# Optimization experiments

Measured on AMD Instinct MI355X. Metric: run time of the kernel, lower is better.

Reference implementation:

```python
import jax, jax.numpy as jnp
import numpy as np

NB, NA, NC, NH, NW = 32, 5, 20, 76, 76
MAXT, NGT_PER_IMG = 50, 12
ANCHORS = [1.3221, 1.73145, 3.19275, 4.00944, 5.05587, 8.09892, 9.47112, 4.84053, 11.2364, 10.0071]
NOOBJ_SCALE, OBJ_SCALE = 1.0, 5.0
COORD_SCALE, CLASS_SCALE = 1.0, 1.0
SIL_THRESH = 0.6


def setup_inputs() -> dict:
    key = jax.random.key(0)
    output = jax.random.normal(key, (NB, NA * (5 + NC), NH, NW), jnp.float32) * 0.5
    rng = np.random.default_rng(0)
    tgt = np.zeros((NB, MAXT * 5), np.float32)
    for b in range(NB):
        # distinct grid cells per image -> scatter order never matters
        cells = rng.choice(NH * NW, size=NGT_PER_IMG, replace=False)
        gj, gi = cells // NW, cells % NW
        tgt[b, 0:NGT_PER_IMG * 5:5] = rng.integers(0, NC, NGT_PER_IMG)
        tgt[b, 1:NGT_PER_IMG * 5:5] = (gi + rng.uniform(0.1, 0.9, NGT_PER_IMG)) / NW
        tgt[b, 2:NGT_PER_IMG * 5:5] = (gj + rng.uniform(0.1, 0.9, NGT_PER_IMG)) / NH
        tgt[b, 3:NGT_PER_IMG * 5:5] = rng.uniform(0.03, 0.3, NGT_PER_IMG)
        tgt[b, 4:NGT_PER_IMG * 5:5] = rng.uniform(0.03, 0.3, NGT_PER_IMG)
    return {"output": output, "target": jnp.asarray(tgt),
            "anchors": jnp.asarray(ANCHORS, jnp.float32)}


def _iou(a, b):
    # boxes (..., 4) in (cx, cy, w, h); matches bbox_iou(x1y1x2y2=False)
    ax, ay, aw, ah = a[..., 0], a[..., 1], a[..., 2], a[..., 3]
    bx, by, bw, bh = b[..., 0], b[..., 1], b[..., 2], b[..., 3]
    uw = jnp.maximum(ax + aw / 2, bx + bw / 2) - jnp.minimum(ax - aw / 2, bx - bw / 2)
    uh = jnp.maximum(ay + ah / 2, by + bh / 2) - jnp.minimum(ay - ah / 2, by - bh / 2)
    cw = aw + bw - uw
    ch = ah + bh - uh
    carea = jnp.where((cw <= 0) | (ch <= 0), 0.0, cw * ch)
    return carea / (aw * ah + bw * bh - carea)


def reference(output, target, anchors):
    nB, _, nH, nW = output.shape
    nA, nC = NA, NC
    T = target.shape[1] // 5
    total = nB * nA * nH * nW

    out = output.reshape(nB, nA, 5 + nC, nH, nW)
    x = jax.nn.sigmoid(out[:, :, 0])          # [nB,nA,nH,nW]
    y = jax.nn.sigmoid(out[:, :, 1])
    w = out[:, :, 2]
    h = out[:, :, 3]
    conf = jax.nn.sigmoid(out[:, :, 4])
    cls_logits = jnp.moveaxis(out[:, :, 5:], 2, -1)  # [nB,nA,nH,nW,nC]

    aw, ah = anchors[0::2], anchors[1::2]     # [nA]
    px = x + jnp.arange(nW, dtype=x.dtype)[None, None, None, :]
    py = y + jnp.arange(nH, dtype=x.dtype)[None, None, :, None]
    pw = jnp.exp(w) * aw[None, :, None, None]
    ph = jnp.exp(h) * ah[None, :, None, None]
    # torch uses .data -> decoded boxes are detached
    pred = jax.lax.stop_gradient(jnp.stack([px, py, pw, ph], -1))  # [nB,nA,nH,nW,4]

    tgt = target.reshape(nB, T, 5)
    cls_t = tgt[..., 0]
    gx, gy = tgt[..., 1] * nW, tgt[..., 2] * nH
    gw, gh = tgt[..., 3] * nW, tgt[..., 4] * nH
    valid = tgt[..., 1] != 0                  # [nB,T] (padding uses x==0)
    gt_boxes = jnp.stack([gx, gy, gw, gh], -1)  # [nB,T,4]

    # --- conf_mask: zero out cells whose best-matching-gt IoU > thresh ---
    ious = _iou(pred[:, :, :, :, None, :], gt_boxes[:, None, None, None, :, :])  # [nB,nA,nH,nW,T]
    max_iou = jnp.max(jnp.where(valid[:, None, None, None, :], ious, 0.0), axis=-1)
    conf_mask = jnp.where(max_iou > SIL_THRESH, 0.0, NOOBJ_SCALE)

    # --- best anchor per gt (shape-only IoU, zero-centered) ---
    abox = jnp.stack([jnp.zeros_like(aw), jnp.zeros_like(ah), aw, ah], -1)  # [nA,4]
    gbox0 = jnp.stack([jnp.zeros_like(gw), jnp.zeros_like(gh), gw, gh], -1)
    aiou = _iou(gbox0[:, :, None, :], abox[None, None, :, :])  # [nB,T,nA]
    best_n = jnp.argmax(aiou, axis=-1)                         # first max == strict > loop

    gi = jnp.clip(gx.astype(jnp.int32), 0, nW - 1)
    gj = jnp.clip(gy.astype(jnp.int32), 0, nH - 1)
    bidx = jnp.arange(nB)[:, None]
    idx = ((bidx * nA + best_n) * nH + gj) * nW + gi
    idx = jnp.where(valid, idx, total)        # invalid -> out of range -> dropped
    idxf = idx.reshape(-1)

    aw_b, ah_b = aw[best_n], ah[best_n]
    tx_v = gx - gi
    ty_v = gy - gj
    tw_v = jnp.log(jnp.where(valid, gw, aw_b) / aw_b)
    th_v = jnp.log(jnp.where(valid, gh, ah_b) / ah_b)
    pred_flat = pred.reshape(total, 4)
    pb = pred_flat[jnp.clip(idx, 0, total - 1)]        # [nB,T,4]
    tconf_v = _iou(gt_boxes, pb)

    def scat(vals):
        return jnp.zeros((total,), x.dtype).at[idxf].set(
            vals.reshape(-1).astype(x.dtype), mode='drop').reshape(nB, nA, nH, nW)

    coord_mask = scat(jnp.ones_like(gx))
    cls_mask = scat(jnp.ones_like(gx))
    tx = scat(tx_v)
    ty = scat(ty_v)
    tw = scat(tw_v)
    th = scat(th_v)
    tconf = scat(tconf_v)
    tcls = scat(cls_t)
    conf_mask = conf_mask.reshape(-1).at[idxf].set(OBJ_SCALE, mode='drop').reshape(nB, nA, nH, nW)
    conf_mask = jnp.sqrt(conf_mask)

    cm = coord_mask
    loss_x = COORD_SCALE * jnp.sum((x * cm - tx * cm) ** 2) / 2.0
    loss_y = COORD_SCALE * jnp.sum((y * cm - ty * cm) ** 2) / 2.0
    loss_w = COORD_SCALE * jnp.sum((w * cm - tw * cm) ** 2) / 2.0
    loss_h = COORD_SCALE * jnp.sum((h * cm - th * cm) ** 2) / 2.0
    loss_conf = jnp.sum((conf * conf_mask - tconf * conf_mask) ** 2) / 2.0

    logp = jax.nn.log_softmax(cls_logits, axis=-1)
    ce = -jnp.take_along_axis(logp, tcls.astype(jnp.int32)[..., None], axis=-1)[..., 0]
    loss_cls = CLASS_SCALE * jnp.sum(ce * cls_mask)

    return (loss_x + loss_y + loss_w + loss_h + loss_conf + loss_cls) / nB
```

## Files before the change

kernel.cpp:

```cpp
#include <hip/hip_runtime.h>
#include <math.h>

#define NB 32
#define NA 5
#define NC 20
#define NH 76
#define NW 76
#define MAXT 50
#define NHW (NH * NW)
#define CH (5 + NC)
#define CELLS_PER_IMG (NA * NHW)
#define NGROUPS (CELLS_PER_IMG / 4)
#define P2_BLOCKS ((NGROUPS + 255) / 256)
#define TOTAL_BLOCKS (P2_BLOCKS * NB)
#define SIL 0.6f

__device__ __forceinline__ float sigmoidf_(float v) {
    return 1.0f / (1.0f + __expf(-v));
}

__global__ __launch_bounds__(256) void yolo_loss_kernel(
    const float* __restrict__ out, const float* __restrict__ target,
    const float* __restrict__ anchors, float* __restrict__ partials)
{
    __shared__ float  s_aw[NA], s_ah[NA];
    __shared__ float4 s_tbox[MAXT];
    __shared__ float  s_thr[MAXT];
    __shared__ float  s_bar[MAXT];
    __shared__ int    s_cell[MAXT];
    __shared__ int    s_cnt;
    __shared__ float  s_part[4];

    const int tid = threadIdx.x;
    const int b   = blockIdx.y;

    if (tid < NA) { s_aw[tid] = anchors[2 * tid]; s_ah[tid] = anchors[2 * tid + 1]; }
    if (tid == 0) s_cnt = 0;
    __syncthreads();

    float lsum = 0.0f;

    if (tid < MAXT) {
        const float* tp = target + (size_t)b * MAXT * 5 + tid * 5;
        float tc = tp[0], xn = tp[1], yn = tp[2], wn = tp[3], hn = tp[4];
        if (xn != 0.0f) {
            float gx = xn * NW, gy = yn * NH, gw = wn * NW, gh = hn * NH;

            int bn = 0; float best = -1.0f;
            #pragma unroll
            for (int a = 0; a < NA; ++a) {
                float mw = fminf(gw, s_aw[a]);
                float mh = fminf(gh, s_ah[a]);
                float car = mw * mh;
                float iou = car / (gw * gh + s_aw[a] * s_ah[a] - car);
                if (iou > best) { best = iou; bn = a; }
            }
            int gi = (int)gx; gi = gi < 0 ? 0 : (gi > NW - 1 ? NW - 1 : gi);
            int gj = (int)gy; gj = gj < 0 ? 0 : (gj > NH - 1 ? NH - 1 : gj);

            int pos = atomicAdd(&s_cnt, 1);
            float barea = gw * gh;
            s_tbox[pos] = make_float4(gx - 0.5f * gw, gy - 0.5f * gh,
                                      gx + 0.5f * gw, gy + 0.5f * gh);
            s_thr[pos]  = 0.375f * barea;
            s_bar[pos]  = barea;
            s_cell[pos] = bn * NHW + gj * NW + gi;

            if (blockIdx.x == 0) {
                float tx = gx - gi, ty = gy - gj;
                float tw = __logf(gw / s_aw[bn]);
                float th = __logf(gh / s_ah[bn]);
                const float* cp = out + ((size_t)(b * NA + bn) * CH) * NHW + gj * NW + gi;
                float xr = sigmoidf_(cp[0]);
                float yr = sigmoidf_(cp[(size_t)1 * NHW]);
                float wr = cp[(size_t)2 * NHW];
                float hr = cp[(size_t)3 * NHW];
                lsum += 0.5f * ((xr - tx) * (xr - tx) + (yr - ty) * (yr - ty) +
                                (wr - tw) * (wr - tw) + (hr - th) * (hr - th));
                int c = (int)tc;
                float lg[NC];
                float m = -1e30f;
                #pragma unroll
                for (int k = 0; k < NC; ++k) {
                    lg[k] = cp[(size_t)(5 + k) * NHW];
                    m = fmaxf(m, lg[k]);
                }
                float s = 0.0f;
                #pragma unroll
                for (int k = 0; k < NC; ++k) s += __expf(lg[k] - m);
                lsum += (m + __logf(s)) - lg[c];
            }
        }
    }
    __syncthreads();

    const int cnt = s_cnt;
    const int g = blockIdx.x * 256 + tid;
    if (g < NGROUPS) {
        const int cell0 = g * 4;
        const int a  = cell0 / NHW;
        const int r  = cell0 - a * NHW;
        const int j  = r / NW;
        const int i0 = r - j * NW;
        const float* cp = out + ((size_t)(b * NA + a) * CH) * NHW + r;
        const float4 vx = *(const float4*)(cp);
        const float4 vy = *(const float4*)(cp + (size_t)1 * NHW);
        const float4 vw = *(const float4*)(cp + (size_t)2 * NHW);
        const float4 vh = *(const float4*)(cp + (size_t)3 * NHW);
        const float4 vc = *(const float4*)(cp + (size_t)4 * NHW);
        const float aw = s_aw[a], ah = s_ah[a];

        const float xs[4] = {vx.x, vx.y, vx.z, vx.w};
        const float ys[4] = {vy.x, vy.y, vy.z, vy.w};
        const float ws[4] = {vw.x, vw.y, vw.z, vw.w};
        const float hs[4] = {vh.x, vh.y, vh.z, vh.w};
        const float cs[4] = {vc.x, vc.y, vc.z, vc.w};

        float pxmin[4], pxmax[4], pymin[4], pymax[4], pthr[4], parea[4];
        float objcar[4], objbar[4];
        bool  ex[4];
        #pragma unroll
        for (int c = 0; c < 4; ++c) {
            float px = sigmoidf_(xs[c]) + (float)(i0 + c);
            float py = sigmoidf_(ys[c]) + (float)j;
            float pw = __expf(ws[c]) * aw;
            float ph = __expf(hs[c]) * ah;
            pxmin[c] = px - 0.5f * pw; pxmax[c] = px + 0.5f * pw;
            pymin[c] = py - 0.5f * ph; pymax[c] = py + 0.5f * ph;
            parea[c] = pw * ph;
            pthr[c]  = 0.375f * parea[c];
            objcar[c] = -1.0f; objbar[c] = 0.0f; ex[c] = false;
        }

        for (int u = 0; u < cnt; ++u) {
            const float4 tb   = s_tbox[u];
            const float  tthr = s_thr[u];
            const float  tbar = s_bar[u];
            const int    tcell = s_cell[u];
            #pragma unroll
            for (int c = 0; c < 4; ++c) {
                float iw  = fminf(pxmax[c], tb.z) - fmaxf(pxmin[c], tb.x);
                float ih  = fminf(pymax[c], tb.w) - fmaxf(pymin[c], tb.y);
                float car = fmaxf(iw, 0.0f) * fmaxf(ih, 0.0f);
                ex[c] = ex[c] | (car > pthr[c] + tthr);
                bool hit = (tcell == cell0 + c);
                objcar[c] = hit ? car  : objcar[c];
                objbar[c] = hit ? tbar : objbar[c];
            }
        }

        #pragma unroll
        for (int c = 0; c < 4; ++c) {
            float conf = sigmoidf_(cs[c]);
            bool  obj  = objcar[c] >= 0.0f;
            float den  = parea[c] + objbar[c] - objcar[c];
            float tcf  = objcar[c] / den;
            float tconf = obj ? tcf : 0.0f;
            float d = conf - tconf;
            float scale = obj ? 5.0f : (ex[c] ? 0.0f : 1.0f);
            lsum += 0.5f * scale * d * d;
        }
    }

    for (int o = 32; o > 0; o >>= 1) lsum += __shfl_down(lsum, o, 64);
    if ((tid & 63) == 0) s_part[tid >> 6] = lsum;
    __syncthreads();
    if (tid == 0) {
        partials[blockIdx.y * P2_BLOCKS + blockIdx.x] =
            s_part[0] + s_part[1] + s_part[2] + s_part[3];
    }
}

__global__ __launch_bounds__(256) void final_reduce_kernel(
    const float* __restrict__ partials, float* __restrict__ loss)
{
    __shared__ float s_part[4];
    const int tid = threadIdx.x;
    float v = 0.0f;
    for (int i = tid; i < TOTAL_BLOCKS; i += 256) v += partials[i];
    for (int o = 32; o > 0; o >>= 1) v += __shfl_down(v, o, 64);
    if ((tid & 63) == 0) s_part[tid >> 6] = v;
    __syncthreads();
    if (tid == 0) loss[0] = (s_part[0] + s_part[1] + s_part[2] + s_part[3]) * (1.0f / NB);
}

extern "C" void kernel_launch(void* const* d_in, const int* in_sizes, int n_in,
                              void* d_out, int out_size, void* d_ws, size_t ws_size,
                              hipStream_t stream) {
    const float* out_p    = (const float*)d_in[0];
    const float* target_p = (const float*)d_in[1];
    const float* anchor_p = (const float*)d_in[2];
    float* loss_p    = (float*)d_out;
    float* partial_p = (float*)d_ws;

    dim3 grid(P2_BLOCKS, NB);
    yolo_loss_kernel<<<grid, dim3(256), 0, stream>>>(out_p, target_p, anchor_p, partial_p);
    final_reduce_kernel<<<dim3(1), dim3(256), 0, stream>>>(partial_p, loss_p);
}
```

Measured before the change: 132.9 us.

## Fuse final reduction via last-block atomic counter and move object conf loss to GT threads

Replaces the separate final reduction kernel with a last-block-done pattern: each block publishes its partial sum, bumps a global counter, and the last block sums all partials. A memset on the counter is added to the stream. The object-cell confidence term is moved out of the per-cell loop into the GT threads of block 0, so the inner loop over targets only updates an exclusion flag and no longer tracks per-cell hit area. This cuts per-cell registers and selects and removes a kernel launch, in exchange for a memset launch and threadfence/atomic overhead.

```diff
diff --git a/kernel.cpp b/kernel.cpp
--- a/kernel.cpp
+++ b/kernel.cpp
@@ -13,29 +13,29 @@
 #define NGROUPS (CELLS_PER_IMG / 4)
 #define P2_BLOCKS ((NGROUPS + 255) / 256)
 #define TOTAL_BLOCKS (P2_BLOCKS * NB)
-#define SIL 0.6f
 
 __device__ __forceinline__ float sigmoidf_(float v) {
     return 1.0f / (1.0f + __expf(-v));
 }
 
-__global__ __launch_bounds__(256) void yolo_loss_kernel(
+__global__ __launch_bounds__(256) void yolo_loss_fused(
     const float* __restrict__ out, const float* __restrict__ target,
-    const float* __restrict__ anchors, float* __restrict__ partials)
+    const float* __restrict__ anchors, float* __restrict__ partials,
+    unsigned* __restrict__ counter, float* __restrict__ loss)
 {
     __shared__ float  s_aw[NA], s_ah[NA];
     __shared__ float4 s_tbox[MAXT];
     __shared__ float  s_thr[MAXT];
-    __shared__ float  s_bar[MAXT];
     __shared__ int    s_cell[MAXT];
     __shared__ int    s_cnt;
     __shared__ float  s_part[4];
+    __shared__ int    s_last;
 
     const int tid = threadIdx.x;
     const int b   = blockIdx.y;
 
     if (tid < NA) { s_aw[tid] = anchors[2 * tid]; s_ah[tid] = anchors[2 * tid + 1]; }
-    if (tid == 0) s_cnt = 0;
+    if (tid == 0) { s_cnt = 0; s_last = 0; }
     __syncthreads();
 
     float lsum = 0.0f;
@@ -58,25 +58,38 @@
             int gi = (int)gx; gi = gi < 0 ? 0 : (gi > NW - 1 ? NW - 1 : gi);
             int gj = (int)gy; gj = gj < 0 ? 0 : (gj > NH - 1 ? NH - 1 : gj);
 
+            float barea = gw * gh;
+            float xmin = gx - 0.5f * gw, ymin = gy - 0.5f * gh;
+            float xmax = gx + 0.5f * gw, ymax = gy + 0.5f * gh;
+
             int pos = atomicAdd(&s_cnt, 1);
-            float barea = gw * gh;
-            s_tbox[pos] = make_float4(gx - 0.5f * gw, gy - 0.5f * gh,
-                                      gx + 0.5f * gw, gy + 0.5f * gh);
+            s_tbox[pos] = make_float4(xmin, ymin, xmax, ymax);
             s_thr[pos]  = 0.375f * barea;
-            s_bar[pos]  = barea;
             s_cell[pos] = bn * NHW + gj * NW + gi;
 
             if (blockIdx.x == 0) {
-                float tx = gx - gi, ty = gy - gj;
-                float tw = __logf(gw / s_aw[bn]);
-                float th = __logf(gh / s_ah[bn]);
                 const float* cp = out + ((size_t)(b * NA + bn) * CH) * NHW + gj * NW + gi;
                 float xr = sigmoidf_(cp[0]);
                 float yr = sigmoidf_(cp[(size_t)1 * NHW]);
                 float wr = cp[(size_t)2 * NHW];
                 float hr = cp[(size_t)3 * NHW];
+                float cr = sigmoidf_(cp[(size_t)4 * NHW]);
+
+                float tx = gx - gi, ty = gy - gj;
+                float tw = __logf(gw / s_aw[bn]);
+                float th = __logf(gh / s_ah[bn]);
                 lsum += 0.5f * ((xr - tx) * (xr - tx) + (yr - ty) * (yr - ty) +
                                 (wr - tw) * (wr - tw) + (hr - th) * (hr - th));
+
+                float px = xr + (float)gi, py = yr + (float)gj;
+                float pw = __expf(wr) * s_aw[bn];
+                float ph = __expf(hr) * s_ah[bn];
+                float iw  = fminf(px + 0.5f * pw, xmax) - fmaxf(px - 0.5f * pw, xmin);
+                float ih  = fminf(py + 0.5f * ph, ymax) - fmaxf(py - 0.5f * ph, ymin);
+                float car = fmaxf(iw, 0.0f) * fmaxf(ih, 0.0f);
+                float tconf = car / (pw * ph + barea - car);
+                lsum += 2.5f * (cr - tconf) * (cr - tconf);
+
                 int c = (int)tc;
                 float lg[NC];
                 float m = -1e30f;
@@ -116,8 +129,7 @@
         const float hs[4] = {vh.x, vh.y, vh.z, vh.w};
         const float cs[4] = {vc.x, vc.y, vc.z, vc.w};
 
-        float pxmin[4], pxmax[4], pymin[4], pymax[4], pthr[4], parea[4];
-        float objcar[4], objbar[4];
+        float pxmin[4], pxmax[4], pymin[4], pymax[4], pthr[4];
         bool  ex[4];
         #pragma unroll
         for (int c = 0; c < 4; ++c) {
@@ -127,38 +139,27 @@
             float ph = __expf(hs[c]) * ah;
             pxmin[c] = px - 0.5f * pw; pxmax[c] = px + 0.5f * pw;
             pymin[c] = py - 0.5f * ph; pymax[c] = py + 0.5f * ph;
-            parea[c] = pw * ph;
-            pthr[c]  = 0.375f * parea[c];
-            objcar[c] = -1.0f; objbar[c] = 0.0f; ex[c] = false;
+            pthr[c]  = 0.375f * (pw * ph);
+            ex[c] = false;
         }
 
         for (int u = 0; u < cnt; ++u) {
-            const float4 tb   = s_tbox[u];
-            const float  tthr = s_thr[u];
-            const float  tbar = s_bar[u];
-            const int    tcell = s_cell[u];
+            const float4 tb    = s_tbox[u];
+            const float  tthr  = s_thr[u];
+            const int    dcell = s_cell[u] - cell0;
             #pragma unroll
             for (int c = 0; c < 4; ++c) {
                 float iw  = fminf(pxmax[c], tb.z) - fmaxf(pxmin[c], tb.x);
                 float ih  = fminf(pymax[c], tb.w) - fmaxf(pymin[c], tb.y);
                 float car = fmaxf(iw, 0.0f) * fmaxf(ih, 0.0f);
-                ex[c] = ex[c] | (car > pthr[c] + tthr);
-                bool hit = (tcell == cell0 + c);
-                objcar[c] = hit ? car  : objcar[c];
-                objbar[c] = hit ? tbar : objbar[c];
+                ex[c] = ex[c] | (car > pthr[c] + tthr) | (dcell == c);
             }
         }
 
         #pragma unroll
         for (int c = 0; c < 4; ++c) {
             float conf = sigmoidf_(cs[c]);
-            bool  obj  = objcar[c] >= 0.0f;
-            float den  = parea[c] + objbar[c] - objcar[c];
-            float tcf  = objcar[c] / den;
-            float tconf = obj ? tcf : 0.0f;
-            float d = conf - tconf;
-            float scale = obj ? 5.0f : (ex[c] ? 0.0f : 1.0f);
-            lsum += 0.5f * scale * d * d;
+            lsum += ex[c] ? 0.0f : 0.5f * conf * conf;
         }
     }
 
@@ -168,20 +169,24 @@
     if (tid == 0) {
         partials[blockIdx.y * P2_BLOCKS + blockIdx.x] =
             s_part[0] + s_part[1] + s_part[2] + s_part[3];
-    }
-}
-
-__global__ __launch_bounds__(256) void final_reduce_kernel(
-    const float* __restrict__ partials, float* __restrict__ loss)
-{
-    __shared__ float s_part[4];
-    const int tid = threadIdx.x;
-    float v = 0.0f;
-    for (int i = tid; i < TOTAL_BLOCKS; i += 256) v += partials[i];
-    for (int o = 32; o > 0; o >>= 1) v += __shfl_down(v, o, 64);
-    if ((tid & 63) == 0) s_part[tid >> 6] = v;
-    __syncthreads();
-    if (tid == 0) loss[0] = (s_part[0] + s_part[1] + s_part[2] + s_part[3]) * (1.0f / NB);
+        __threadfence();
+        unsigned t = atomicAdd(counter, 1u);
+        s_last = (t == TOTAL_BLOCKS - 1) ? 1 : 0;
+    }
+    __syncthreads();
+
+    if (s_last) {
+        __threadfence();
+        float v = 0.0f;
+        for (int i = tid; i < TOTAL_BLOCKS; i += 256)
+            v += __hip_atomic_load(&partials[i], __ATOMIC_RELAXED,
+                                   __HIP_MEMORY_SCOPE_AGENT);
+        for (int o = 32; o > 0; o >>= 1) v += __shfl_down(v, o, 64);
+        if ((tid & 63) == 0) s_part[tid >> 6] = v;
+        __syncthreads();
+        if (tid == 0)
+            loss[0] = (s_part[0] + s_part[1] + s_part[2] + s_part[3]) * (1.0f / NB);
+    }
 }
 
 extern "C" void kernel_launch(void* const* d_in, const int* in_sizes, int n_in,
@@ -190,10 +195,14 @@
     const float* out_p    = (const float*)d_in[0];
     const float* target_p = (const float*)d_in[1];
     const float* anchor_p = (const float*)d_in[2];
-    float* loss_p    = (float*)d_out;
-    float* partial_p = (float*)d_ws;
+    float* loss_p = (float*)d_out;
+
+    unsigned* counter_p = (unsigned*)d_ws;
+    float*    partial_p = (float*)d_ws + 256;
+
+    hipMemsetAsync(counter_p, 0, sizeof(unsigned), stream);
 
     dim3 grid(P2_BLOCKS, NB);
-    yolo_loss_kernel<<<grid, dim3(256), 0, stream>>>(out_p, target_p, anchor_p, partial_p);
-    final_reduce_kernel<<<dim3(1), dim3(256), 0, stream>>>(partial_p, loss_p);
+    yolo_loss_fused<<<grid, dim3(256), 0, stream>>>(out_p, target_p, anchor_p,
+                                                    partial_p, counter_p, loss_p);
 }
```

Result: slower. 151.3 us (+13.8%).
